# Kernel tuning notes

Measured on AMD Instinct MI355X. Metric: run time of the kernel, lower is better.

## Reference

```python
import jax, jax.numpy as jnp
import numpy as np

D_MODEL = 2048
NUM_HEADS = 16
D_K = D_MODEL // NUM_HEADS
THETA = 10000.0
MAX_SEQ_LEN = 2048
B, S = 2, 2048


def setup_inputs() -> dict:
    key = jax.random.key(0)
    ks = jax.random.split(key, 5)
    x = jax.random.normal(ks[0], (B, S, D_MODEL), dtype=jnp.float32)
    token_positions = jnp.tile(jnp.arange(S, dtype=jnp.int64 if jax.config.jax_enable_x64 else jnp.int32), (B, 1))
    wq = jax.random.normal(ks[1], (D_MODEL, D_MODEL), dtype=jnp.float32)
    wk = jax.random.normal(ks[2], (D_MODEL, D_MODEL), dtype=jnp.float32)
    wv = jax.random.normal(ks[3], (D_MODEL, D_MODEL), dtype=jnp.float32)
    wo = jax.random.normal(ks[4], (D_MODEL, D_MODEL), dtype=jnp.float32)
    return {"x": x, "token_positions": token_positions, "wq": wq, "wk": wk, "wv": wv, "wo": wo}


def _rope_tables():
    # inv freqs: exp(arange(0,d_k,2) * (-log(theta)/d_k))  -> [d_k/2]
    inv_freq = jnp.exp(jnp.arange(0, D_K, 2, dtype=jnp.float32) * (-np.log(THETA) / D_K))
    m = jnp.arange(MAX_SEQ_LEN, dtype=jnp.float32)[:, None]  # [L,1]
    ang = m * inv_freq[None, :]                               # [L, d_k/2]
    return jnp.cos(ang), jnp.sin(ang)


def _apply_rope(x, token_positions, cos_tab, sin_tab):
    # x: [B, H, S, d_k]; token_positions: [B, S]
    cos = cos_tab[token_positions][:, None, :, :]  # [B,1,S,d_k/2]
    sin = sin_tab[token_positions][:, None, :, :]
    xe = x[..., 0::2]
    xo = x[..., 1::2]
    re = xe * cos - xo * sin
    ro = xo * cos + xe * sin
    out = jnp.stack([re, ro], axis=-1).reshape(x.shape)
    return out


def reference(x, token_positions, wq, wk, wv, wo):
    b, s, _ = x.shape
    cos_tab, sin_tab = _rope_tables()

    def split_heads(t):  # [B,S,D] -> [B,H,S,d_k]
        return t.reshape(b, s, NUM_HEADS, D_K).transpose(0, 2, 1, 3)

    q = _apply_rope(split_heads(x @ wq), token_positions, cos_tab, sin_tab)
    k = _apply_rope(split_heads(x @ wk), token_positions, cos_tab, sin_tab)
    v = split_heads(x @ wv)

    scores = jnp.einsum("bhqd,bhkd->bhqk", q, k) / jnp.sqrt(jnp.float32(D_K))
    causal = jnp.tril(jnp.ones((s, s), dtype=bool))
    scores = jnp.where(causal[None, None], scores, jnp.float32(-1e9))
    attn = jax.nn.softmax(scores, axis=-1)
    out = jnp.einsum("bhqk,bhkd->bhqd", attn, v)
    out = out.transpose(0, 2, 1, 3).reshape(b, s, D_MODEL)
    return out @ wo
```

## Files before the change

### kernel.cpp

```cpp
#include <hip/hip_runtime.h>
#include <hip/hip_bf16.h>
#include <cstdio>

namespace {

constexpr int kSeq = 2048;
constexpr int kDModel = 2048;
constexpr int kHeads = 16;
constexpr int kDk = 128;
constexpr int kBatch = 2;
constexpr int kM = kBatch * kSeq;
constexpr float kQScale = 0.08838834764831845f;

typedef __bf16 bf16_t;
typedef __bf16 bf16x8 __attribute__((ext_vector_type(8)));
typedef __bf16 bf16x4 __attribute__((ext_vector_type(4)));
typedef float f32x4 __attribute__((ext_vector_type(4)));
typedef short s16x4 __attribute__((ext_vector_type(4)));

__device__ __forceinline__ f32x4 mfma32(bf16x8 a, bf16x8 b, f32x4 c) {
  return __builtin_amdgcn_mfma_f32_16x16x32_bf16(a, b, c, 0, 0, 0);
}

#if __has_builtin(__builtin_amdgcn_mfma_f32_16x16x16_bf16)
__device__ __forceinline__ f32x4 mfma16(bf16x4 a, bf16x4 b, f32x4 c) {
  return __builtin_amdgcn_mfma_f32_16x16x16_bf16(a, b, c, 0, 0, 0);
}
#else
__device__ __forceinline__ f32x4 mfma16(bf16x4 a, bf16x4 b, f32x4 c) {
  union U { bf16x4 b; s16x4 s; } ua, ub;
  ua.b = a; ub.b = b;
  return __builtin_amdgcn_mfma_f32_16x16x16bf16_1k(ua.s, ub.s, c, 0, 0, 0);
}
#endif

using gas_void = const __attribute__((address_space(1))) void;
using las_void = __attribute__((address_space(3))) void;

__device__ __forceinline__ void gload_lds16(const bf16_t* g, bf16_t* l) {
  __builtin_amdgcn_global_load_lds((gas_void*)g, (las_void*)l, 16, 0, 0);
}

__global__ void k_rope_table(float* __restrict__ cost, float* __restrict__ sint) {
  const int p = blockIdx.x;
  const int i = threadIdx.x;
  const double inv = exp(-(double)(2 * i) * 9.210340371976184 / 128.0);
  const double ang = (double)p * inv;
  cost[p * 64 + i] = (float)cos(ang);
  sint[p * 64 + i] = (float)sin(ang);
}

__global__ void k_split_x(const float* __restrict__ x, bf16_t* __restrict__ xh,
                          bf16_t* __restrict__ xl, int n) {
  const int idx = (blockIdx.x * blockDim.x + threadIdx.x) * 4;
  if (idx >= n) return;
  const float4 v = *(const float4*)(x + idx);
  const float vv[4] = {v.x, v.y, v.z, v.w};
  bf16x4 hv, lv;
#pragma unroll
  for (int j = 0; j < 4; ++j) {
    const bf16_t h = (bf16_t)vv[j];
    hv[j] = h;
    lv[j] = (bf16_t)(vv[j] - (float)h);
  }
  *(bf16x4*)(xh + idx) = hv;
  *(bf16x4*)(xl + idx) = lv;
}

__global__ void k_transpose_w(const float* __restrict__ w, bf16_t* __restrict__ wth,
                              bf16_t* __restrict__ wtl) {
  __shared__ float tile[32][33];
  const int bx = blockIdx.x * 32;
  const int by = blockIdx.y * 32;
  const int tx = threadIdx.x, ty = threadIdx.y;
#pragma unroll
  for (int i = 0; i < 32; i += 8)
    tile[ty + i][tx] = w[(size_t)(by + ty + i) * kDModel + bx + tx];
  __syncthreads();
#pragma unroll
  for (int i = 0; i < 32; i += 8) {
    const float v = tile[tx][ty + i];
    const size_t o = (size_t)(bx + ty + i) * kDModel + by + tx;
    const bf16_t h = (bf16_t)v;
    wth[o] = h;
    if (wtl) wtl[o] = (bf16_t)(v - (float)h);
  }
}

__global__ __launch_bounds__(512) void k_gemmf(
    const bf16_t* __restrict__ Ah, const bf16_t* __restrict__ Al,
    const bf16_t* __restrict__ Bh, const bf16_t* __restrict__ Bl,
    bf16_t* __restrict__ Qh, bf16_t* __restrict__ Ql,
    bf16_t* __restrict__ Kh, bf16_t* __restrict__ Kl,
    const int* __restrict__ tokpos, const float* __restrict__ cost,
    const float* __restrict__ sint) {
  __shared__ __align__(16) bf16_t sA[4][256 * 32];
  __shared__ __align__(16) bf16_t sB[4][256 * 32];
  constexpr int ntk = 192;

  const int tid = threadIdx.x;
  const int wid = tid >> 6, lane = tid & 63;
  const int lo = lane & 15, hi = lane >> 4;
  const int wr = wid >> 2;
  const int wc = wid & 3;

  const int bid = blockIdx.x;
  const int wgid = (bid & 7) * 32 + (bid >> 3);
  const int m0 = (wgid >> 4) * 256, n0 = (wgid & 15) * 256;

  const int sr = tid >> 2;
  const int sc = ((tid & 3) ^ ((tid >> 3) & 3)) * 8;
  size_t offA[2], offB[2];
#pragma unroll
  for (int i = 0; i < 2; ++i) {
    offA[i] = (size_t)(m0 + i * 128 + sr) * 2048 + sc;
    offB[i] = (size_t)(n0 + i * 128 + sr) * 2048 + sc;
  }

  auto STAGE_A = [&](int slot, int tt) {
    const bf16_t* As = (tt < 128) ? Ah : Al;
    const int kb = (tt & 63) * 32;
#pragma unroll
    for (int i = 0; i < 2; ++i)
      gload_lds16(As + offA[i] + kb, sA[slot] + i * 4096 + tid * 8);
  };
  auto STAGE_B = [&](int slot, int tt) {
    const bf16_t* Bs = (tt < 64) ? Bh : ((tt < 128) ? Bl : Bh);
    const int kb = (tt & 63) * 32;
#pragma unroll
    for (int i = 0; i < 2; ++i)
      gload_lds16(Bs + offB[i] + kb, sB[slot] + i * 4096 + tid * 8);
  };

  const int xq = (lo >> 1) & 3;
  int aoff[8], boff[4];
#pragma unroll
  for (int mi = 0; mi < 8; ++mi)
    aoff[mi] = (wr * 128 + mi * 16 + lo) * 32 + ((hi ^ xq) * 8);
#pragma unroll
  for (int ni = 0; ni < 4; ++ni)
    boff[ni] = (wc * 64 + ni * 16 + lo) * 32 + ((hi ^ xq) * 8);

  f32x4 acc[8][4];
  const f32x4 z = {0.f, 0.f, 0.f, 0.f};
#pragma unroll
  for (int i = 0; i < 8; ++i)
#pragma unroll
    for (int j = 0; j < 4; ++j) acc[i][j] = z;

  STAGE_A(0, 0);
  STAGE_B(0, 0);
  STAGE_A(1, 1);
  STAGE_B(1, 1);
  STAGE_A(2, 2);
  STAGE_B(2, 2);
  asm volatile("s_waitcnt vmcnt(8)" ::: "memory");
  __builtin_amdgcn_s_barrier();
  __builtin_amdgcn_sched_barrier(0);

  int s0 = 0;
#pragma unroll 1
  for (int t = 0; t < ntk; ++t) {
    const bf16_t* sa = sA[s0];
    const bf16_t* sb = sB[s0];
    const int s3 = (s0 + 3) & 3;
    const bool pf = (t + 3 < ntk);

    bf16x8 a[4], b[4];
#pragma unroll
    for (int mi = 0; mi < 4; ++mi) a[mi] = *(const bf16x8*)(sa + aoff[mi]);
#pragma unroll
    for (int ni = 0; ni < 4; ++ni) b[ni] = *(const bf16x8*)(sb + boff[ni]);
    if (pf) STAGE_A(s3, t + 3);
    __builtin_amdgcn_sched_barrier(0);
    __builtin_amdgcn_s_barrier();
    asm volatile("s_waitcnt lgkmcnt(0)" ::: "memory");
    __builtin_amdgcn_sched_barrier(0);
    __builtin_amdgcn_s_setprio(1);
#pragma unroll
    for (int ni = 0; ni < 4; ++ni)
#pragma unroll
      for (int mi = 0; mi < 4; ++mi)
        acc[mi][ni] = mfma32(a[mi], b[ni], acc[mi][ni]);
    __builtin_amdgcn_s_setprio(0);
    __builtin_amdgcn_sched_barrier(0);
    __builtin_amdgcn_s_barrier();
    __builtin_amdgcn_sched_barrier(0);

    bf16x8 a2[4];
#pragma unroll
    for (int mi = 0; mi < 4; ++mi) a2[mi] = *(const bf16x8*)(sa + aoff[4 + mi]);
    if (pf) STAGE_B(s3, t + 3);
    __builtin_amdgcn_sched_barrier(0);
    if (t <= ntk - 4)
      asm volatile("s_waitcnt vmcnt(8)" ::: "memory");
    else if (t == ntk - 3)
      asm volatile("s_waitcnt vmcnt(4)" ::: "memory");
    else if (t == ntk - 2)
      asm volatile("s_waitcnt vmcnt(0)" ::: "memory");
    __builtin_amdgcn_s_barrier();
    asm volatile("s_waitcnt lgkmcnt(0)" ::: "memory");
    __builtin_amdgcn_sched_barrier(0);
    __builtin_amdgcn_s_setprio(1);
#pragma unroll
    for (int ni = 0; ni < 4; ++ni)
#pragma unroll
      for (int mi = 0; mi < 4; ++mi)
        acc[4 + mi][ni] = mfma32(a2[mi], b[ni], acc[4 + mi][ni]);
    __builtin_amdgcn_s_setprio(0);
    __builtin_amdgcn_sched_barrier(0);
    __builtin_amdgcn_s_barrier();
    __builtin_amdgcn_sched_barrier(0);

    s0 = (s0 + 1) & 3;
  }

  const int qk = n0 >> 11;
  bf16_t* Xh = qk ? Kh : Qh;
  bf16_t* Xl = qk ? Kl : Ql;
  const float scale = qk ? 1.0f : kQScale;
  const int is64 = (tokpos[1] == 0) ? 1 : 0;
#pragma unroll
  for (int mi = 0; mi < 8; ++mi) {
#pragma unroll
    for (int r = 0; r < 4; ++r) {
      const int row = m0 + wr * 128 + mi * 16 + hi * 4 + r;
      const int pos = is64 ? tokpos[2 * row] : tokpos[row];
#pragma unroll
      for (int ni = 0; ni < 4; ++ni) {
        const int col = n0 + wc * 64 + ni * 16 + lo;
        const float v = acc[mi][ni][r] * scale;
        const float pv = __shfl_xor(v, 1);
        const int ip = (col & 127) >> 1;
        const float c = cost[pos * 64 + ip];
        const float sn = sint[pos * 64 + ip];
        const float sgn = (lo & 1) ? sn : -sn;
        const float rv = v * c + pv * sgn;
        const bf16_t hb = (bf16_t)rv;
        const size_t o = (size_t)row * 2048 + (col & 2047);
        Xh[o] = hb;
        Xl[o] = (bf16_t)(rv - (float)hb);
      }
    }
  }
}

template <int EPI>
__global__ __launch_bounds__(512) void k_gemmvo(
    const bf16_t* __restrict__ Ah, const bf16_t* __restrict__ Bh,
    void* __restrict__ O0) {
  __shared__ __align__(16) bf16_t sA[3][256 * 32];
  __shared__ __align__(16) bf16_t sB[3][128 * 32];
  constexpr int ntk = 64;

  const int tid = threadIdx.x;
  const int wid = tid >> 6, lane = tid & 63;
  const int lo = lane & 15, hi = lane >> 4;
  const int wrr = wid >> 1;
  const int wcc = wid & 1;

  const int bid = blockIdx.x;
  const int wgid = (bid & 7) * 32 + (bid >> 3);
  const int m0 = (wgid >> 4) * 256, n0 = (wgid & 15) * 128;

  const int sr = tid >> 2;
  const int sc = ((tid & 3) ^ ((tid >> 3) & 3)) * 8;
  size_t offA[2];
#pragma unroll
  for (int i = 0; i < 2; ++i)
    offA[i] = (size_t)(m0 + i * 128 + sr) * 2048 + sc;
  const size_t offB = (size_t)(n0 + sr) * 2048 + sc;

  auto STAGE = [&](int slot, int tt) {
    const int kb = tt * 32;
#pragma unroll
    for (int i = 0; i < 2; ++i)
      gload_lds16(Ah + offA[i] + kb, sA[slot] + i * 4096 + tid * 8);
    gload_lds16(Bh + offB + kb, sB[slot] + tid * 8);
  };

  const int xq = (lo >> 1) & 3;
  int aoff[4], boff[4];
#pragma unroll
  for (int mi = 0; mi < 4; ++mi)
    aoff[mi] = (wrr * 64 + mi * 16 + lo) * 32 + ((hi ^ xq) * 8);
#pragma unroll
  for (int ni = 0; ni < 4; ++ni)
    boff[ni] = (wcc * 64 + ni * 16 + lo) * 32 + ((hi ^ xq) * 8);

  f32x4 acc[4][4];
  const f32x4 z = {0.f, 0.f, 0.f, 0.f};
#pragma unroll
  for (int i = 0; i < 4; ++i)
#pragma unroll
    for (int j = 0; j < 4; ++j) acc[i][j] = z;

  STAGE(0, 0);
  STAGE(1, 1);
  asm volatile("s_waitcnt vmcnt(3)" ::: "memory");
  __builtin_amdgcn_s_barrier();
  __builtin_amdgcn_sched_barrier(0);

  int s0 = 0;
#pragma unroll 1
  for (int t = 0; t < ntk; ++t) {
    const bf16_t* sa = sA[s0];
    const bf16_t* sb = sB[s0];
    int s2 = s0 + 2;
    if (s2 >= 3) s2 -= 3;

    bf16x8 a[4], b[4];
#pragma unroll
    for (int mi = 0; mi < 4; ++mi) a[mi] = *(const bf16x8*)(sa + aoff[mi]);
#pragma unroll
    for (int ni = 0; ni < 4; ++ni) b[ni] = *(const bf16x8*)(sb + boff[ni]);
    if (t + 2 < ntk) STAGE(s2, t + 2);
    __builtin_amdgcn_sched_barrier(0);
    if (t + 3 < ntk)
      asm volatile("s_waitcnt vmcnt(3)" ::: "memory");
    else if (t == ntk - 2)
      asm volatile("s_waitcnt vmcnt(0)" ::: "memory");
    __builtin_amdgcn_s_barrier();
    asm volatile("s_waitcnt lgkmcnt(0)" ::: "memory");
    __builtin_amdgcn_sched_barrier(0);
    __builtin_amdgcn_s_setprio(1);
#pragma unroll
    for (int ni = 0; ni < 4; ++ni)
#pragma unroll
      for (int mi = 0; mi < 4; ++mi)
        acc[mi][ni] = mfma32(a[mi], b[ni], acc[mi][ni]);
    __builtin_amdgcn_s_setprio(0);
    __builtin_amdgcn_sched_barrier(0);
    __builtin_amdgcn_s_barrier();
    __builtin_amdgcn_sched_barrier(0);

    s0 += 1;
    if (s0 >= 3) s0 = 0;
  }

  if constexpr (EPI == 0) {
    float* C = (float*)O0;
#pragma unroll
    for (int mi = 0; mi < 4; ++mi)
#pragma unroll
      for (int ni = 0; ni < 4; ++ni)
#pragma unroll
        for (int r = 0; r < 4; ++r) {
          const int row = m0 + wrr * 64 + mi * 16 + hi * 4 + r;
          const int col = n0 + wcc * 64 + ni * 16 + lo;
          C[(size_t)row * 2048 + col] = acc[mi][ni][r];
        }
  } else {
    bf16_t* VT = (bf16_t*)O0;
#pragma unroll
    for (int mi = 0; mi < 4; ++mi)
#pragma unroll
      for (int ni = 0; ni < 4; ++ni) {
        const int col = n0 + wcc * 64 + ni * 16 + lo;
        const int h = col >> 7, d = col & 127;
        const int rowb = m0 + wrr * 64 + mi * 16 + hi * 4;
        const int b = rowb >> 11, s = rowb & (kSeq - 1);
        bf16x4 ov;
#pragma unroll
        for (int r = 0; r < 4; ++r) ov[r] = (bf16_t)acc[mi][ni][r];
        *(bf16x4*)(VT + ((size_t)((b * kHeads + h) * kDk + d)) * kSeq + s) = ov;
      }
  }
}

__global__ __launch_bounds__(512, 2) void k_attn4(
    const bf16_t* __restrict__ Qh, const bf16_t* __restrict__ Ql,
    const bf16_t* __restrict__ Kh, const bf16_t* __restrict__ Kl,
    const bf16_t* __restrict__ VT, bf16_t* __restrict__ Ob) {
  __shared__ __align__(16) bf16_t sK[2][2][64 * 128];
  __shared__ __align__(16) bf16_t sV[2][128 * 64];

  const int tid = threadIdx.x;
  const int wid = tid >> 6, lane = tid & 63;
  const int lo = lane & 15, hi = lane >> 4;
  const int flat = blockIdx.x;
  const int j = flat >> 3;
  const int bh = (flat & 7) * 4 + (j & 3);
  const int p = j >> 2;
  const int b = bh >> 4, h = bh & 15;
  const int qiW = (wid < 4) ? (15 - p) : p;
  const int qw = qiW * 128 + (wid & 3) * 32;
  const int nkv = 2 * (15 - p) + 2;

  bf16x8 qhf[4][2], qlf[4][2];
  {
    const size_t qbase =
        (size_t)(b * kSeq + qw + lo) * kDModel + h * kDk + hi * 8;
#pragma unroll
    for (int qt = 0; qt < 2; ++qt)
#pragma unroll
      for (int ks = 0; ks < 4; ++ks) {
        const size_t o = qbase + (size_t)qt * 16 * kDModel + ks * 32;
        qhf[ks][qt] = *(const bf16x8*)(Qh + o);
        qlf[ks][qt] = *(const bf16x8*)(Ql + o);
      }
  }

  const int rK0 = wid * 8 + (lane >> 4);
  const int gK0 = ((lane & 15) ^ (rK0 & 15)) * 8;
  const int gK1 = ((lane & 15) ^ ((rK0 + 4) & 15)) * 8;
  const bf16_t* pKh0 = Kh + (size_t)(b * kSeq + rK0) * kDModel + h * kDk + gK0;
  const bf16_t* pKh1 = Kh + (size_t)(b * kSeq + rK0 + 4) * kDModel + h * kDk + gK1;
  const bf16_t* pKl0 = Kl + (pKh0 - Kh);
  const bf16_t* pKl1 = Kl + (pKh1 - Kh);
  const int dV0 = wid * 16 + (lane >> 3);
  const int gV0 = ((lane & 7) ^ (dV0 & 7)) * 8;
  const int gV1 = ((lane & 7) ^ ((dV0 + 8) & 7)) * 8;
  const bf16_t* pV0 = VT + (size_t)(bh * kDk + dV0) * kSeq + gV0;
  const bf16_t* pV1 = VT + (size_t)(bh * kDk + dV0 + 8) * kSeq + gV1;
  const int ldsK = (wid * 8) * 128;
  const int ldsV = (wid * 16) * 64;

  f32x4 of[8][2];
  const f32x4 z = {0.f, 0.f, 0.f, 0.f};
#pragma unroll
  for (int di = 0; di < 8; ++di) {
    of[di][0] = z;
    of[di][1] = z;
  }
  float m[2] = {-3e38f, -3e38f};
  float l[2] = {0.f, 0.f};

  auto STAGE = [&](int buf, int t) {
    const size_t ko = (size_t)t * 64 * kDModel;
    const size_t vo = (size_t)t * 64;
    bf16_t* dk = sK[buf][0] + ldsK;
    bf16_t* dl = sK[buf][1] + ldsK;
    gload_lds16(pKh0 + ko, dk);
    gload_lds16(pKh1 + ko, dk + 512);
    gload_lds16(pKl0 + ko, dl);
    gload_lds16(pKl1 + ko, dl + 512);
    bf16_t* dv = sV[buf] + ldsV;
    gload_lds16(pV0 + vo, dv);
    gload_lds16(pV1 + vo, dv + 512);
  };

  STAGE(0, 0);
  __syncthreads();

  for (int t = 0; t < nkv; ++t) {
    const int kv0 = t * 64;
    if (t + 1 < nkv) STAGE((t + 1) & 1, t + 1);

    if (kv0 <= qw + 31) {
      const bf16_t* bKh = sK[t & 1][0];
      const bf16_t* bKl = sK[t & 1][1];
      const bf16_t* bV = sV[t & 1];
      const bool maskedw = (kv0 + 63 > qw);

      f32x4 st[4][2];
#pragma unroll
      for (int kt = 0; kt < 4; ++kt) {
        st[kt][0] = z;
        st[kt][1] = z;
      }
#pragma unroll
      for (int kt = 0; kt < 4; ++kt) {
#pragma unroll
        for (int ks = 0; ks < 4; ++ks) {
          const int krow = kt * 16 + lo;
          const int ka = krow * 128 + (((ks * 4 + hi) ^ (krow & 15)) * 8);
          const bf16x8 kh8 = *(const bf16x8*)(bKh + ka);
          const bf16x8 kl8 = *(const bf16x8*)(bKl + ka);
#pragma unroll
          for (int qt = 0; qt < 2; ++qt) {
            st[kt][qt] = mfma32(kh8, qhf[ks][qt], st[kt][qt]);
            st[kt][qt] = mfma32(kh8, qlf[ks][qt], st[kt][qt]);
            st[kt][qt] = mfma32(kl8, qhf[ks][qt], st[kt][qt]);
          }
        }
      }

      bf16x4 pb[4][2];
#pragma unroll
      for (int qt = 0; qt < 2; ++qt) {
        const int q = qw + qt * 16 + lo;
        float mt = -3e38f;
#pragma unroll
        for (int kt = 0; kt < 4; ++kt)
#pragma unroll
          for (int r = 0; r < 4; ++r) {
            float s = st[kt][qt][r];
            if (maskedw && (kv0 + kt * 16 + hi * 4 + r > q)) s = -1e30f;
            st[kt][qt][r] = s;
            mt = fmaxf(mt, s);
          }
        mt = fmaxf(mt, __shfl_xor(mt, 16));
        mt = fmaxf(mt, __shfl_xor(mt, 32));
        if (!__all(mt <= m[qt] + 8.f)) {
          const float mnew = fmaxf(m[qt], mt);
          const float corr = __expf(m[qt] - mnew);
          l[qt] *= corr;
#pragma unroll
          for (int di = 0; di < 8; ++di) of[di][qt] = of[di][qt] * corr;
          m[qt] = mnew;
        }
        float rs = 0.f;
#pragma unroll
        for (int kt = 0; kt < 4; ++kt) {
          bf16x4 pv;
#pragma unroll
          for (int r = 0; r < 4; ++r) {
            const float pp = __expf(st[kt][qt][r] - m[qt]);
            rs += pp;
            pv[r] = (bf16_t)pp;
          }
          pb[kt][qt] = pv;
        }
        rs += __shfl_xor(rs, 16);
        rs += __shfl_xor(rs, 32);
        l[qt] += rs;
      }

#pragma unroll
      for (int di = 0; di < 8; ++di) {
        const int d = di * 16 + lo;
#pragma unroll
        for (int kt = 0; kt < 4; ++kt) {
          const int va =
              d * 64 + (((kt * 2 + (hi >> 1)) ^ (d & 7)) * 8) + (hi & 1) * 4;
          const bf16x4 vf = *(const bf16x4*)(bV + va);
          of[di][0] = mfma16(vf, pb[kt][0], of[di][0]);
          of[di][1] = mfma16(vf, pb[kt][1], of[di][1]);
        }
      }
    }
    __syncthreads();
  }

#pragma unroll
  for (int qt = 0; qt < 2; ++qt) {
    const float linv = 1.f / l[qt];
    const size_t ob =
        (size_t)(b * kSeq + qw + qt * 16 + lo) * kDModel + h * kDk + hi * 4;
#pragma unroll
    for (int di = 0; di < 8; ++di) {
      bf16x4 ov;
#pragma unroll
      for (int r = 0; r < 4; ++r) ov[r] = (bf16_t)(of[di][qt][r] * linv);
      *(bf16x4*)(Ob + ob + di * 16) = ov;
    }
  }
}

}

extern "C" void kernel_launch(void* const* d_in, const int* in_sizes, int n_in,
                              void* d_out, int out_size, void* d_ws, size_t ws_size,
                              hipStream_t stream) {
  (void)in_sizes; (void)n_in; (void)out_size;
  const float* x = (const float*)d_in[0];
  const int* tokpos = (const int*)d_in[1];
  const float* wq = (const float*)d_in[2];
  const float* wk = (const float*)d_in[3];
  const float* wv = (const float*)d_in[4];
  const float* wo = (const float*)d_in[5];
  float* out = (float*)d_out;

  char* p = (char*)d_ws;
  auto take = [&](size_t bytes) { char* q = p; p += bytes; return q; };
  float* cost = (float*)take((size_t)kSeq * 64 * sizeof(float));
  float* sint = (float*)take((size_t)kSeq * 64 * sizeof(float));
  const size_t mat = (size_t)kM * kDModel * sizeof(bf16_t);
  const size_t wmat = (size_t)kDModel * kDModel * sizeof(bf16_t);
  bf16_t* xh = (bf16_t*)take(mat);
  bf16_t* xl = (bf16_t*)take(mat);
  bf16_t* wqkth = (bf16_t*)take(2 * wmat);
  bf16_t* wqktl = (bf16_t*)take(2 * wmat);
  bf16_t* wvt = (bf16_t*)take(wmat);
  bf16_t* wot = (bf16_t*)take(wmat);
  bf16_t* qh = (bf16_t*)take(mat);
  bf16_t* ql = (bf16_t*)take(mat);
  bf16_t* kh = (bf16_t*)take(mat);
  bf16_t* kl = (bf16_t*)take(mat);
  bf16_t* vt = (bf16_t*)take(mat);
  bf16_t* ob = (bf16_t*)take(mat);
  if ((size_t)(p - (char*)d_ws) > ws_size) {
    fprintf(stderr, "MHA: workspace too small: need %zu have %zu\n",
            (size_t)(p - (char*)d_ws), ws_size);
    return;
  }

  k_rope_table<<<dim3(kSeq), dim3(64), 0, stream>>>(cost, sint);
  k_split_x<<<dim3((kM * kDModel) / (256 * 4)), dim3(256), 0, stream>>>(
      x, xh, xl, kM * kDModel);
  {
    dim3 tb(32, 8), tg(kDModel / 32, kDModel / 32);
    k_transpose_w<<<tg, tb, 0, stream>>>(wq, wqkth, wqktl);
    k_transpose_w<<<tg, tb, 0, stream>>>(wk, wqkth + (size_t)2048 * 2048,
                                         wqktl + (size_t)2048 * 2048);
    k_transpose_w<<<tg, tb, 0, stream>>>(wv, wvt, nullptr);
    k_transpose_w<<<tg, tb, 0, stream>>>(wo, wot, nullptr);
  }
  k_gemmf<<<dim3(256), dim3(512), 0, stream>>>(xh, xl, wqkth, wqktl, qh, ql,
                                               kh, kl, tokpos, cost, sint);
  k_gemmvo<2><<<dim3(256), dim3(512), 0, stream>>>(xh, wvt, vt);
  k_attn4<<<dim3(256), dim3(512), 0, stream>>>(qh, ql, kh, kl, vt, ob);
  k_gemmvo<0><<<dim3(256), dim3(512), 0, stream>>>(ob, wot, out);
}
```

Measured before the change: 432.7 us.

## Give each attention wave two 16-row query slices from paired tiles for balance

Each wave in the attention kernel used to own 32 consecutive query rows, either from the late tile (waves 0-3) or the early tile (waves 4-7), so half the waves sat idle through most KV iterations. Now every wave takes one 16-row slice from the late tile and one from the early tile, and the MFMA work for the early slice is skipped once it passes the causal limit. The aim is to balance causal work across the eight waves so none idles at the block barrier. In exchange there are more per-slice branches and masking checks, and the early-slice MFMAs are issued under a runtime condition.

```diff
diff --git a/kernel.cpp b/kernel.cpp
--- a/kernel.cpp
+++ b/kernel.cpp
@@ -368,7 +368,7 @@
   }
 }
 
-__global__ __launch_bounds__(512, 2) void k_attn4(
+__global__ __launch_bounds__(512, 2) void k_attn5(
     const bf16_t* __restrict__ Qh, const bf16_t* __restrict__ Ql,
     const bf16_t* __restrict__ Kh, const bf16_t* __restrict__ Kl,
     const bf16_t* __restrict__ VT, bf16_t* __restrict__ Ob) {
@@ -383,22 +383,21 @@
   const int bh = (flat & 7) * 4 + (j & 3);
   const int p = j >> 2;
   const int b = bh >> 4, h = bh & 15;
-  const int qiW = (wid < 4) ? (15 - p) : p;
-  const int qw = qiW * 128 + (wid & 3) * 32;
+  const int qs0 = (15 - p) * 128 + wid * 16;
+  const int qs1 = p * 128 + wid * 16;
   const int nkv = 2 * (15 - p) + 2;
 
   bf16x8 qhf[4][2], qlf[4][2];
-  {
+#pragma unroll
+  for (int s = 0; s < 2; ++s) {
+    const int qs = s ? qs1 : qs0;
     const size_t qbase =
-        (size_t)(b * kSeq + qw + lo) * kDModel + h * kDk + hi * 8;
-#pragma unroll
-    for (int qt = 0; qt < 2; ++qt)
-#pragma unroll
-      for (int ks = 0; ks < 4; ++ks) {
-        const size_t o = qbase + (size_t)qt * 16 * kDModel + ks * 32;
-        qhf[ks][qt] = *(const bf16x8*)(Qh + o);
-        qlf[ks][qt] = *(const bf16x8*)(Ql + o);
-      }
+        (size_t)(b * kSeq + qs + lo) * kDModel + h * kDk + hi * 8;
+#pragma unroll
+    for (int ks = 0; ks < 4; ++ks) {
+      qhf[ks][s] = *(const bf16x8*)(Qh + qbase + ks * 32);
+      qlf[ks][s] = *(const bf16x8*)(Ql + qbase + ks * 32);
+    }
   }
 
   const int rK0 = wid * 8 + (lane >> 4);
@@ -447,11 +446,12 @@
     const int kv0 = t * 64;
     if (t + 1 < nkv) STAGE((t + 1) & 1, t + 1);
 
-    if (kv0 <= qw + 31) {
+    const bool actA = (kv0 <= qs0 + 15);
+    const bool actB = (kv0 <= qs1 + 15);
+    if (actA) {
       const bf16_t* bKh = sK[t & 1][0];
       const bf16_t* bKl = sK[t & 1][1];
       const bf16_t* bV = sV[t & 1];
-      const bool maskedw = (kv0 + 63 > qw);
 
       f32x4 st[4][2];
 #pragma unroll
@@ -467,38 +467,43 @@
           const int ka = krow * 128 + (((ks * 4 + hi) ^ (krow & 15)) * 8);
           const bf16x8 kh8 = *(const bf16x8*)(bKh + ka);
           const bf16x8 kl8 = *(const bf16x8*)(bKl + ka);
-#pragma unroll
-          for (int qt = 0; qt < 2; ++qt) {
-            st[kt][qt] = mfma32(kh8, qhf[ks][qt], st[kt][qt]);
-            st[kt][qt] = mfma32(kh8, qlf[ks][qt], st[kt][qt]);
-            st[kt][qt] = mfma32(kl8, qhf[ks][qt], st[kt][qt]);
+          st[kt][0] = mfma32(kh8, qhf[ks][0], st[kt][0]);
+          st[kt][0] = mfma32(kh8, qlf[ks][0], st[kt][0]);
+          st[kt][0] = mfma32(kl8, qhf[ks][0], st[kt][0]);
+          if (actB) {
+            st[kt][1] = mfma32(kh8, qhf[ks][1], st[kt][1]);
+            st[kt][1] = mfma32(kh8, qlf[ks][1], st[kt][1]);
+            st[kt][1] = mfma32(kl8, qhf[ks][1], st[kt][1]);
           }
         }
       }
 
       bf16x4 pb[4][2];
 #pragma unroll
-      for (int qt = 0; qt < 2; ++qt) {
-        const int q = qw + qt * 16 + lo;
+      for (int s = 0; s < 2; ++s) {
+        if (s == 1 && !actB) continue;
+        const int qs = s ? qs1 : qs0;
+        const int q = qs + lo;
+        const bool masked = (kv0 + 63 > qs);
         float mt = -3e38f;
 #pragma unroll
         for (int kt = 0; kt < 4; ++kt)
 #pragma unroll
           for (int r = 0; r < 4; ++r) {
-            float s = st[kt][qt][r];
-            if (maskedw && (kv0 + kt * 16 + hi * 4 + r > q)) s = -1e30f;
-            st[kt][qt][r] = s;
-            mt = fmaxf(mt, s);
+            float v = st[kt][s][r];
+            if (masked && (kv0 + kt * 16 + hi * 4 + r > q)) v = -1e30f;
+            st[kt][s][r] = v;
+            mt = fmaxf(mt, v);
           }
         mt = fmaxf(mt, __shfl_xor(mt, 16));
         mt = fmaxf(mt, __shfl_xor(mt, 32));
-        if (!__all(mt <= m[qt] + 8.f)) {
-          const float mnew = fmaxf(m[qt], mt);
-          const float corr = __expf(m[qt] - mnew);
-          l[qt] *= corr;
-#pragma unroll
-          for (int di = 0; di < 8; ++di) of[di][qt] = of[di][qt] * corr;
-          m[qt] = mnew;
+        if (!__all(mt <= m[s] + 8.f)) {
+          const float mnew = fmaxf(m[s], mt);
+          const float corr = __expf(m[s] - mnew);
+          l[s] *= corr;
+#pragma unroll
+          for (int di = 0; di < 8; ++di) of[di][s] = of[di][s] * corr;
+          m[s] = mnew;
         }
         float rs = 0.f;
 #pragma unroll
@@ -506,15 +511,15 @@
           bf16x4 pv;
 #pragma unroll
           for (int r = 0; r < 4; ++r) {
-            const float pp = __expf(st[kt][qt][r] - m[qt]);
+            const float pp = __expf(st[kt][s][r] - m[s]);
             rs += pp;
             pv[r] = (bf16_t)pp;
           }
-          pb[kt][qt] = pv;
+          pb[kt][s] = pv;
         }
         rs += __shfl_xor(rs, 16);
         rs += __shfl_xor(rs, 32);
-        l[qt] += rs;
+        l[s] += rs;
       }
 
 #pragma unroll
@@ -526,7 +531,7 @@
               d * 64 + (((kt * 2 + (hi >> 1)) ^ (d & 7)) * 8) + (hi & 1) * 4;
           const bf16x4 vf = *(const bf16x4*)(bV + va);
           of[di][0] = mfma16(vf, pb[kt][0], of[di][0]);
-          of[di][1] = mfma16(vf, pb[kt][1], of[di][1]);
+          if (actB) of[di][1] = mfma16(vf, pb[kt][1], of[di][1]);
         }
       }
     }
@@ -534,15 +539,16 @@
   }
 
 #pragma unroll
-  for (int qt = 0; qt < 2; ++qt) {
-    const float linv = 1.f / l[qt];
+  for (int s = 0; s < 2; ++s) {
+    const int qs = s ? qs1 : qs0;
+    const float linv = 1.f / l[s];
     const size_t ob =
-        (size_t)(b * kSeq + qw + qt * 16 + lo) * kDModel + h * kDk + hi * 4;
+        (size_t)(b * kSeq + qs + lo) * kDModel + h * kDk + hi * 4;
 #pragma unroll
     for (int di = 0; di < 8; ++di) {
       bf16x4 ov;
 #pragma unroll
-      for (int r = 0; r < 4; ++r) ov[r] = (bf16_t)(of[di][qt][r] * linv);
+      for (int r = 0; r < 4; ++r) ov[r] = (bf16_t)(of[di][s][r] * linv);
       *(bf16x4*)(Ob + ob + di * 16) = ov;
     }
   }
@@ -600,6 +606,6 @@
   k_gemmf<<<dim3(256), dim3(512), 0, stream>>>(xh, xl, wqkth, wqktl, qh, ql,
                                                kh, kl, tokpos, cost, sint);
   k_gemmvo<2><<<dim3(256), dim3(512), 0, stream>>>(xh, wvt, vt);
-  k_attn4<<<dim3(256), dim3(512), 0, stream>>>(qh, ql, kh, kl, vt, ob);
+  k_attn5<<<dim3(256), dim3(512), 0, stream>>>(qh, ql, kh, kl, vt, ob);
   k_gemmvo<0><<<dim3(256), dim3(512), 0, stream>>>(ob, wot, out);
 }
```

After: 459.8 us. 6.3% more time.
